# Kernel tuning notes

Hardware: AMD Instinct MI355X
Metric: run time of the kernel (lower is better)

The kernel has to match this reference:

```python
import jax, jax.numpy as jnp
import numpy as np

N, K, D, V = 20000, 16, 256, 64  # nodes, neighbors, embed_dim, edge vocab


def setup_inputs() -> dict:
    key = jax.random.key(0)
    ks = jax.random.split(key, 16)
    s = 1.0 / np.sqrt(2 * D)  # Linear(512 -> 256) init scale
    return {
        "node_reps": jax.random.normal(ks[0], (1, N, D), jnp.float32),
        "in_indices": jax.random.randint(ks[1], (1, N, K), 0, N, jnp.int32),
        "in_edges": jax.random.randint(ks[2], (1, N, K), 0, V, jnp.int32),
        "in_mask": jax.random.uniform(ks[3], (1, N, K), jnp.float32),
        "out_indices": jax.random.randint(ks[4], (1, N, K), 0, N, jnp.int32),
        "out_edges": jax.random.randint(ks[5], (1, N, K), 0, V, jnp.int32),
        "out_mask": jax.random.uniform(ks[6], (1, N, K), jnp.float32),
        "edge_emb_1": jax.random.normal(ks[7], (V, D), jnp.float32),
        "W_1": jax.random.uniform(ks[8], (2 * D, D), jnp.float32, -s, s),
        "b_1": jnp.zeros((D,), jnp.float32),
        "edge_emb_2": jax.random.normal(ks[9], (V, D), jnp.float32),
        "W_2": jax.random.uniform(ks[10], (2 * D, D), jnp.float32, -s, s),
        "b_2": jnp.zeros((D,), jnp.float32),
        "edge_emb_3": jax.random.normal(ks[11], (V, D), jnp.float32),
        "W_3": jax.random.uniform(ks[12], (2 * D, D), jnp.float32, -s, s),
        "b_3": jnp.zeros((D,), jnp.float32),
    }


def gcn_layer(node_reps, in_idx, in_edg, in_msk, out_idx, out_edg, out_msk,
              edge_emb, W, b):
    # node_reps: [1, N, D]; dropout is identity in eval mode.
    nodes = node_reps[0]  # [N, D]; batch_size == 1 as in the original repo

    def agg(idx, edg, msk):
        nbr = nodes[idx]          # gather: [1, N, K, D]
        erep = edge_emb[edg]      # embedding lookup: [1, N, K, D]
        reps = jnp.concatenate([nbr, erep], axis=3) * msk[..., None]
        return reps.sum(axis=2)   # masked sum over neighbors: [1, N, 2D]

    in_reps = agg(in_idx, in_edg, in_msk)
    out_reps = agg(out_idx, out_edg, out_msk)
    in_nodes = in_reps[0] @ W + b    # [N, D]
    out_nodes = out_reps[0] @ W + b  # [N, D]
    return node_reps + out_nodes + in_nodes  # broadcast -> [1, N, D]


def reference(node_reps, in_indices, in_edges, in_mask,
              out_indices, out_edges, out_mask,
              edge_emb_1, W_1, b_1, edge_emb_2, W_2, b_2, edge_emb_3, W_3, b_3):
    nbrs = (in_indices, in_edges, in_mask, out_indices, out_edges, out_mask)
    hidden = gcn_layer(node_reps, *nbrs, edge_emb_1, W_1, b_1)  # gc1
    mu = gcn_layer(hidden, *nbrs, edge_emb_2, W_2, b_2)          # gc2
    logvar = gcn_layer(hidden, *nbrs, edge_emb_3, W_3, b_3)      # gc3

    mu_t = jnp.tanh(mu[0])        # [N, D]
    lv_t = jnp.tanh(logvar[0])    # [N, D]
    n_nodes = mu_t.shape[0]
    kld = (-0.5 / n_nodes) * jnp.mean(
        jnp.sum(1.0 + 2.0 * lv_t - mu_t ** 2 - jnp.exp(lv_t) ** 2, axis=1))
    return hidden, kld
```

## Files before the change

kernel.cpp:

```cpp
#include <hip/hip_runtime.h>
#include <math.h>

#define NN 20000
#define KK 16
#define DD 256
#define VV 64
#define NT1 16
#define SAS 336
#define SAS8 336

typedef __attribute__((ext_vector_type(8))) __bf16 bf16x8;
typedef __attribute__((ext_vector_type(4))) float floatx4;
typedef __attribute__((ext_vector_type(2))) float floatx2;
typedef __attribute__((ext_vector_type(8))) unsigned short ushort8;

__device__ __forceinline__ float4 ld4(const float* p) { return *reinterpret_cast<const float4*>(p); }

__device__ __forceinline__ unsigned short f2bf(float f) {
    union { float f; unsigned u; } v; v.f = f;
    unsigned r = v.u + 0x7FFFu + ((v.u >> 16) & 1u);
    return (unsigned short)(r >> 16);
}
__device__ __forceinline__ float bf2f(unsigned short u) {
    union { unsigned u; float f; } v; v.u = ((unsigned)u) << 16;
    return v.f;
}
__device__ __forceinline__ unsigned char f2q(float f) {
    return (unsigned char)(__builtin_amdgcn_cvt_pk_fp8_f32(f, 0.f, 0u, false) & 0xFFu);
}
__device__ __forceinline__ float q2f(unsigned char q) {
    floatx2 r = __builtin_amdgcn_cvt_pk_f32_fp8((unsigned)q, false);
    return r.x;
}
__device__ __forceinline__ float ftanh(float v) {
    float e = __expf(2.f * v);
    return 1.f - 2.f * __builtin_amdgcn_rcpf(e + 1.f);
}

__global__ __launch_bounds__(256) void setup(
    const int* __restrict__ ie, const float* __restrict__ im,
    const int* __restrict__ oe, const float* __restrict__ om,
    const float* __restrict__ x,
    const float* __restrict__ e1, const float* __restrict__ W1,
    const float* __restrict__ e2, const float* __restrict__ W2,
    const float* __restrict__ e3, const float* __restrict__ W3,
    unsigned short* __restrict__ U1, unsigned char* __restrict__ U23,
    unsigned short* __restrict__ Hc, unsigned char* __restrict__ Hc8,
    unsigned short* __restrict__ xh) {
    int blk = blockIdx.x, tid = threadIdx.x;
    if (blk < 120) {
        int u1path = blk < 40;
        int NT = u1path ? 16 : 32;
        int g = (u1path ? blk : blk - 40) * 256 + tid;
        int lane = g & 63, ntk = g >> 6;
        int nt = ntk % NT, kt = ntk / NT;
        if (kt >= 10) return;
        int n = nt * 16 + (lane & 15);
        int kbase = kt * 32 + (lane >> 4) * 8;
        const float* W; const float* emb;
        if (u1path)       { W = W1; emb = e1; }
        else if (n < 256) { W = W2; emb = e2; }
        else              { W = W3; emb = e3; n -= 256; }
        float vals[8];
        if (kbase < 256) {
            #pragma unroll
            for (int j = 0; j < 8; ++j) vals[j] = W[(size_t)(kbase + j) * DD + n];
        } else {
            int vb = kbase - 256;
            #pragma unroll
            for (int z = 0; z < 8; ++z) vals[z] = 0.f;
            #pragma unroll 4
            for (int j = 0; j < 256; ++j) {
                float wv = W[(size_t)(256 + j) * DD + n];
                #pragma unroll
                for (int z = 0; z < 8; ++z) vals[z] += emb[(vb + z) * DD + j] * wv;
            }
        }
        if (u1path) {
            unsigned short o8[8];
            #pragma unroll
            for (int j = 0; j < 8; ++j) o8[j] = f2bf(vals[j]);
            *reinterpret_cast<uint4*>(&U1[(size_t)g * 8]) = *reinterpret_cast<uint4*>(o8);
        } else {
            unsigned char o8[8];
            #pragma unroll
            for (int j = 0; j < 8; ++j) o8[j] = f2q(vals[j]);
            *reinterpret_cast<uint2*>(&U23[(size_t)g * 8]) = *reinterpret_cast<uint2*>(o8);
        }
    } else {
        int pb = blk - 120;
        int w = tid >> 6, lane = tid & 63;
        int n = pb * 4 + w;
        int e = 0; float m = 0.f;
        if (lane < 16)      { e = ie[n * KK + lane];      m = im[n * KK + lane]; }
        else if (lane < 32) { e = oe[n * KK + lane - 16]; m = om[n * KK + lane - 16]; }
        float h = 0.f;
        #pragma unroll
        for (int j = 0; j < 32; ++j) {
            int ev = __shfl(e, j);
            float mv = __shfl(m, j);
            if (ev == lane) h += mv;
        }
        Hc [(size_t)n * 64 + lane] = f2bf(h);
        Hc8[(size_t)n * 64 + lane] = f2q(h);
        size_t base = (size_t)pb * 1024 + tid * 4;
        float4 v = ld4(x + base);
        ushort4 o; o.x = f2bf(v.x); o.y = f2bf(v.y); o.z = f2bf(v.z); o.w = f2bf(v.w);
        *reinterpret_cast<ushort4*>(xh + base) = o;
    }
}

__global__ __launch_bounds__(256) void fmm1(const unsigned short* __restrict__ xh, const unsigned short* __restrict__ Hc,
                                            const int* __restrict__ ii, const float* __restrict__ im,
                                            const int* __restrict__ oi, const float* __restrict__ om,
                                            const unsigned short* __restrict__ U, const float* __restrict__ b,
                                            float* __restrict__ out, unsigned char* __restrict__ h8) {
    __shared__ unsigned short sA[16 * SAS];
    __shared__ int sidx[16][32];
    __shared__ float smsk[16][32];
    int n0 = blockIdx.x * 16;
    int tid = threadIdx.x;
    for (int q = tid; q < 512; q += 256) {
        int r = q >> 5, j = q & 31;
        int n = n0 + r;
        sidx[r][j] = (j < 16) ? ii[n * KK + j] : oi[n * KK + j - 16];
        smsk[r][j] = (j < 16) ? im[n * KK + j] : om[n * KK + j - 16];
    }
    if (tid < 128) {
        int r = tid >> 3, k8 = tid & 7;
        *reinterpret_cast<uint4*>(&sA[r * SAS + 256 + k8 * 8]) =
            *reinterpret_cast<const uint4*>(&Hc[(size_t)(n0 + r) * 64 + k8 * 8]);
    }
    __syncthreads();
    int lane = tid & 63, w = tid >> 6;
    int half = lane >> 5, c = (lane & 31) * 8;
    #pragma unroll
    for (int rr = 0; rr < 4; ++rr) {
        int row = w * 4 + rr;
        float acc[8] = {0.f, 0.f, 0.f, 0.f, 0.f, 0.f, 0.f, 0.f};
        #pragma unroll
        for (int j = 0; j < 16; ++j) {
            int j2 = j * 2 + half;
            int idx = sidx[row][j2];
            float m = smsk[row][j2];
            ushort8 u = *reinterpret_cast<const ushort8*>(xh + (size_t)idx * DD + c);
            #pragma unroll
            for (int z = 0; z < 8; ++z) acc[z] += m * bf2f(u[z]);
        }
        #pragma unroll
        for (int z = 0; z < 8; ++z) acc[z] += __shfl_xor(acc[z], 32);
        if (half == 0) {
            unsigned short o8[8];
            #pragma unroll
            for (int z = 0; z < 8; ++z) o8[z] = f2bf(acc[z]);
            *reinterpret_cast<uint4*>(&sA[row * SAS + c]) = *reinterpret_cast<uint4*>(o8);
        }
    }
    __syncthreads();
    int lr = lane & 15, quad = lane >> 4;
    float xp[4][4], bb[4];
    #pragma unroll
    for (int t = 0; t < 4; ++t) {
        int col = (w * 4 + t) * 16 + lr;
        bb[t] = 2.f * b[col];
        #pragma unroll
        for (int r = 0; r < 4; ++r)
            xp[t][r] = bf2f(xh[(size_t)(n0 + quad * 4 + r) * DD + col]);
    }
    floatx4 z = {0.f, 0.f, 0.f, 0.f};
    floatx4 acc[4] = {z, z, z, z};
    for (int kt = 0; kt < 10; ++kt) {
        bf16x8 a = *reinterpret_cast<const bf16x8*>(&sA[lr * SAS + kt * 32 + quad * 8]);
        #pragma unroll
        for (int t = 0; t < 4; ++t) {
            bf16x8 bf = *reinterpret_cast<const bf16x8*>(&U[(size_t)((kt * NT1 + w * 4 + t) * 64 + lane) * 8]);
            acc[t] = __builtin_amdgcn_mfma_f32_16x16x32_bf16(a, bf, acc[t], 0, 0, 0);
        }
    }
    #pragma unroll
    for (int t = 0; t < 4; ++t) {
        int col = (w * 4 + t) * 16 + lr;
        #pragma unroll
        for (int r = 0; r < 4; ++r) {
            size_t o = (size_t)(n0 + quad * 4 + r) * DD + col;
            float v = xp[t][r] + bb[t] + acc[t][r];
            out[o] = v;
            h8[o] = f2q(v);
        }
    }
}

__global__ __launch_bounds__(256) void fmm23(const unsigned char* __restrict__ h8, const unsigned char* __restrict__ Hc8,
                                             const int* __restrict__ ii, const float* __restrict__ im,
                                             const int* __restrict__ oi, const float* __restrict__ om,
                                             const unsigned char* __restrict__ U, const float* __restrict__ b2,
                                             const float* __restrict__ b3, float* __restrict__ kld) {
    __shared__ unsigned char sA[16 * SAS8];
    __shared__ int sidx[16][32];
    __shared__ float smsk[16][32];
    __shared__ float red[4];
    int n0 = blockIdx.x * 16;
    int tid = threadIdx.x;
    for (int q = tid; q < 512; q += 256) {
        int r = q >> 5, j = q & 31;
        int n = n0 + r;
        sidx[r][j] = (j < 16) ? ii[n * KK + j] : oi[n * KK + j - 16];
        smsk[r][j] = (j < 16) ? im[n * KK + j] : om[n * KK + j - 16];
    }
    if (tid < 128) {
        int r = tid >> 3, k8 = tid & 7;
        *reinterpret_cast<uint2*>(&sA[r * SAS8 + 256 + k8 * 8]) =
            *reinterpret_cast<const uint2*>(&Hc8[(size_t)(n0 + r) * 64 + k8 * 8]);
    }
    __syncthreads();
    int lane = tid & 63, w = tid >> 6;
    int g = lane >> 4, cl = lane & 15;
    #pragma unroll
    for (int rr = 0; rr < 4; ++rr) {
        int row = w * 4 + rr;
        float acc[16];
        #pragma unroll
        for (int z = 0; z < 16; ++z) acc[z] = 0.f;
        #pragma unroll
        for (int j = 0; j < 8; ++j) {
            int r = g * 8 + j;
            int idx = sidx[row][r];
            float m = smsk[row][r];
            uint4 u = *reinterpret_cast<const uint4*>(h8 + (size_t)idx * DD + cl * 16);
            unsigned dw[4] = {u.x, u.y, u.z, u.w};
            #pragma unroll
            for (int d = 0; d < 4; ++d) {
                floatx2 f01 = __builtin_amdgcn_cvt_pk_f32_fp8(dw[d], false);
                floatx2 f23 = __builtin_amdgcn_cvt_pk_f32_fp8(dw[d], true);
                acc[d * 4 + 0] += m * f01.x; acc[d * 4 + 1] += m * f01.y;
                acc[d * 4 + 2] += m * f23.x; acc[d * 4 + 3] += m * f23.y;
            }
        }
        #pragma unroll
        for (int z = 0; z < 16; ++z) {
            acc[z] += __shfl_xor(acc[z], 16);
            acc[z] += __shfl_xor(acc[z], 32);
        }
        if (g == 0) {
            unsigned char o16[16];
            #pragma unroll
            for (int z = 0; z < 16; ++z) o16[z] = f2q(acc[z]);
            *reinterpret_cast<uint4*>(&sA[row * SAS8 + cl * 16]) = *reinterpret_cast<uint4*>(o16);
        }
    }
    __syncthreads();
    int lr = lane & 15, quad = lane >> 4;
    float hp[4][4], bm[4], bl[4];
    #pragma unroll
    for (int t = 0; t < 4; ++t) {
        int col = (w * 4 + t) * 16 + lr;
        bm[t] = 2.f * b2[col];
        bl[t] = 2.f * b3[col];
        #pragma unroll
        for (int r = 0; r < 4; ++r)
            hp[t][r] = q2f(h8[(size_t)(n0 + quad * 4 + r) * DD + col]);
    }
    floatx4 z = {0.f, 0.f, 0.f, 0.f};
    floatx4 am[4] = {z, z, z, z};
    floatx4 al[4] = {z, z, z, z};
    for (int kt = 0; kt < 10; ++kt) {
        long a = *reinterpret_cast<const long*>(&sA[lr * SAS8 + kt * 32 + quad * 8]);
        #pragma unroll
        for (int t = 0; t < 4; ++t) {
            int nt = w * 4 + t;
            long bmu = *reinterpret_cast<const long*>(&U[(size_t)((kt * 32 + nt) * 64 + lane) * 8]);
            long blv = *reinterpret_cast<const long*>(&U[(size_t)((kt * 32 + 16 + nt) * 64 + lane) * 8]);
            am[t] = __builtin_amdgcn_mfma_f32_16x16x32_fp8_fp8(a, bmu, am[t], 0, 0, 0);
            al[t] = __builtin_amdgcn_mfma_f32_16x16x32_fp8_fp8(a, blv, al[t], 0, 0, 0);
        }
    }
    float kacc = 0.f;
    #pragma unroll
    for (int t = 0; t < 4; ++t) {
        #pragma unroll
        for (int r = 0; r < 4; ++r) {
            float h = hp[t][r];
            float tm = ftanh(h + bm[t] + am[t][r]);
            float tl = ftanh(h + bl[t] + al[t][r]);
            kacc += (1.f - tm * tm) + (2.f * tl - __expf(2.f * tl));
        }
    }
    #pragma unroll
    for (int off = 32; off > 0; off >>= 1) kacc += __shfl_xor(kacc, off);
    if (lane == 0) red[w] = kacc;
    __syncthreads();
    if (tid == 0)
        atomicAdd(kld, (red[0] + red[1] + red[2] + red[3]) * (-0.5f / ((float)NN * (float)NN)));
}

extern "C" void kernel_launch(void* const* d_in, const int* in_sizes, int n_in,
                              void* d_out, int out_size, void* d_ws, size_t ws_size,
                              hipStream_t stream) {
    const float* x  = (const float*)d_in[0];
    const int*   ii = (const int*)d_in[1];
    const int*   ie = (const int*)d_in[2];
    const float* im = (const float*)d_in[3];
    const int*   oi = (const int*)d_in[4];
    const int*   oe = (const int*)d_in[5];
    const float* om = (const float*)d_in[6];
    const float* e1 = (const float*)d_in[7];
    const float* W1 = (const float*)d_in[8];
    const float* b1 = (const float*)d_in[9];
    const float* e2 = (const float*)d_in[10];
    const float* W2 = (const float*)d_in[11];
    const float* b2 = (const float*)d_in[12];
    const float* e3 = (const float*)d_in[13];
    const float* W3 = (const float*)d_in[14];
    const float* b3 = (const float*)d_in[15];
    float* out = (float*)d_out;

    char* ws = (char*)d_ws;
    unsigned short* U1  = (unsigned short*)(ws);
    unsigned char*  U23 = (unsigned char*)(ws + 163840);
    unsigned short* Hc  = (unsigned short*)(ws + 327680);
    unsigned char*  Hc8 = (unsigned char*)(ws + 2887680);
    unsigned short* xh  = (unsigned short*)(ws + 4167680);
    unsigned char*  h8  = (unsigned char*)(ws + 14407680);

    hipMemsetAsync(out + (size_t)NN * DD, 0, 4, stream);
    setup<<<120 + NN / 4, 256, 0, stream>>>(ie, im, oe, om, x, e1, W1, e2, W2, e3, W3,
                                            U1, U23, Hc, Hc8, xh);
    fmm1 <<<NN / 16, 256, 0, stream>>>(xh, Hc, ii, im, oi, om, U1, b1, out, h8);
    fmm23<<<NN / 16, 256, 0, stream>>>(h8, Hc8, ii, im, oi, om, U23, b2, b3,
                                       out + (size_t)NN * DD);
}
```

Measured before the change: 202.0 us.

## Split fused gather+GEMM into column-chunked aggregation kernels and separate 32-row MFMA kernels

Splits each fused gather-then-GEMM kernel into two launches. The first is an aggregation kernel that gathers neighbor rows in column chunks, so each block touches only a slice of the feature table, and writes a bf16 aggregate buffer. The second is a GEMM kernel that processes 32 rows per block and reuses each B fragment across two M tiles. Layers 2/3 switch from fp8 to bf16 for the aggregate and weights, and nontemporal loads/stores are used for the intermediates. This aims to improve cache locality of the random gathers and MFMA reuse, at the cost of extra kernel launches and a round trip of the aggregate buffer through global memory.

```diff
diff --git a/kernel.cpp b/kernel.cpp
--- a/kernel.cpp
+++ b/kernel.cpp
@@ -5,14 +5,14 @@
 #define KK 16
 #define DD 256
 #define VV 64
-#define NT1 16
 #define SAS 336
-#define SAS8 336
 
 typedef __attribute__((ext_vector_type(8))) __bf16 bf16x8;
 typedef __attribute__((ext_vector_type(4))) float floatx4;
 typedef __attribute__((ext_vector_type(2))) float floatx2;
 typedef __attribute__((ext_vector_type(8))) unsigned short ushort8;
+typedef __attribute__((ext_vector_type(4))) unsigned int uint4v;
+typedef __attribute__((ext_vector_type(2))) unsigned int uint2v;
 
 __device__ __forceinline__ float4 ld4(const float* p) { return *reinterpret_cast<const float4*>(p); }
 
@@ -44,9 +44,8 @@
     const float* __restrict__ e1, const float* __restrict__ W1,
     const float* __restrict__ e2, const float* __restrict__ W2,
     const float* __restrict__ e3, const float* __restrict__ W3,
-    unsigned short* __restrict__ U1, unsigned char* __restrict__ U23,
-    unsigned short* __restrict__ Hc, unsigned char* __restrict__ Hc8,
-    unsigned short* __restrict__ xh) {
+    unsigned short* __restrict__ U1, unsigned short* __restrict__ U23,
+    unsigned short* __restrict__ Sb, unsigned short* __restrict__ xh) {
     int blk = blockIdx.x, tid = threadIdx.x;
     if (blk < 120) {
         int u1path = blk < 40;
@@ -76,17 +75,11 @@
                 for (int z = 0; z < 8; ++z) vals[z] += emb[(vb + z) * DD + j] * wv;
             }
         }
-        if (u1path) {
-            unsigned short o8[8];
-            #pragma unroll
-            for (int j = 0; j < 8; ++j) o8[j] = f2bf(vals[j]);
-            *reinterpret_cast<uint4*>(&U1[(size_t)g * 8]) = *reinterpret_cast<uint4*>(o8);
-        } else {
-            unsigned char o8[8];
-            #pragma unroll
-            for (int j = 0; j < 8; ++j) o8[j] = f2q(vals[j]);
-            *reinterpret_cast<uint2*>(&U23[(size_t)g * 8]) = *reinterpret_cast<uint2*>(o8);
-        }
+        unsigned short o8[8];
+        #pragma unroll
+        for (int j = 0; j < 8; ++j) o8[j] = f2bf(vals[j]);
+        unsigned short* U = u1path ? U1 : U23;
+        *reinterpret_cast<uint4v*>(&U[(size_t)g * 8]) = *reinterpret_cast<uint4v*>(o8);
     } else {
         int pb = blk - 120;
         int w = tid >> 6, lane = tid & 63;
@@ -101,8 +94,7 @@
             float mv = __shfl(m, j);
             if (ev == lane) h += mv;
         }
-        Hc [(size_t)n * 64 + lane] = f2bf(h);
-        Hc8[(size_t)n * 64 + lane] = f2q(h);
+        Sb[(size_t)n * 320 + 256 + lane] = f2bf(h);
         size_t base = (size_t)pb * 1024 + tid * 4;
         float4 v = ld4(x + base);
         ushort4 o; o.x = f2bf(v.x); o.y = f2bf(v.y); o.z = f2bf(v.z); o.w = f2bf(v.w);
@@ -110,179 +102,203 @@
     }
 }
 
-__global__ __launch_bounds__(256) void fmm1(const unsigned short* __restrict__ xh, const unsigned short* __restrict__ Hc,
+__global__ __launch_bounds__(256) void aggx(const unsigned short* __restrict__ xh,
                                             const int* __restrict__ ii, const float* __restrict__ im,
                                             const int* __restrict__ oi, const float* __restrict__ om,
-                                            const unsigned short* __restrict__ U, const float* __restrict__ b,
-                                            float* __restrict__ out, unsigned char* __restrict__ h8) {
-    __shared__ unsigned short sA[16 * SAS];
-    __shared__ int sidx[16][32];
-    __shared__ float smsk[16][32];
-    int n0 = blockIdx.x * 16;
+                                            unsigned short* __restrict__ Sb) {
+    int blk = blockIdx.x;
+    int chunk = blk / 2500, nb = blk % 2500;
+    int w = threadIdx.x >> 6, lane = threadIdx.x & 63;
+    int na = nb * 8 + w * 2, nbod = na + 1;
+    int rg = lane >> 3, co = lane & 7;
+    const unsigned short* base = xh + chunk * 64 + co * 8;
+    float acc[2][8];
+    #pragma unroll
+    for (int s = 0; s < 2; ++s)
+        #pragma unroll
+        for (int z = 0; z < 8; ++z) acc[s][z] = 0.f;
+    #pragma unroll
+    for (int s = 0; s < 2; ++s) {
+        int n = s ? nbod : na;
+        int i0 = ii[n * KK + rg], i1 = ii[n * KK + rg + 8];
+        int i2 = oi[n * KK + rg], i3 = oi[n * KK + rg + 8];
+        float m0 = im[n * KK + rg], m1 = im[n * KK + rg + 8];
+        float m2 = om[n * KK + rg], m3 = om[n * KK + rg + 8];
+        ushort8 u0 = *reinterpret_cast<const ushort8*>(base + (size_t)i0 * DD);
+        ushort8 u1 = *reinterpret_cast<const ushort8*>(base + (size_t)i1 * DD);
+        ushort8 u2 = *reinterpret_cast<const ushort8*>(base + (size_t)i2 * DD);
+        ushort8 u3 = *reinterpret_cast<const ushort8*>(base + (size_t)i3 * DD);
+        #pragma unroll
+        for (int z = 0; z < 8; ++z)
+            acc[s][z] = m0 * bf2f(u0[z]) + m1 * bf2f(u1[z]) + m2 * bf2f(u2[z]) + m3 * bf2f(u3[z]);
+    }
+    #pragma unroll
+    for (int s = 0; s < 2; ++s)
+        #pragma unroll
+        for (int z = 0; z < 8; ++z) {
+            acc[s][z] += __shfl_xor(acc[s][z], 8);
+            acc[s][z] += __shfl_xor(acc[s][z], 16);
+            acc[s][z] += __shfl_xor(acc[s][z], 32);
+        }
+    if (rg < 2) {
+        int n = rg ? nbod : na;
+        unsigned short o8[8];
+        #pragma unroll
+        for (int z = 0; z < 8; ++z) o8[z] = f2bf(acc[rg][z]);
+        __builtin_nontemporal_store(*reinterpret_cast<uint4v*>(o8),
+            reinterpret_cast<uint4v*>(&Sb[(size_t)n * 320 + chunk * 64 + co * 8]));
+    }
+}
+
+__global__ __launch_bounds__(256) void aggq(const unsigned char* __restrict__ h8,
+                                            const int* __restrict__ ii, const float* __restrict__ im,
+                                            const int* __restrict__ oi, const float* __restrict__ om,
+                                            unsigned short* __restrict__ Sb) {
+    int blk = blockIdx.x;
+    int chunk = blk / 2500, nb = blk % 2500;
+    int w = threadIdx.x >> 6, lane = threadIdx.x & 63;
+    int na = nb * 8 + w * 2, nbod = na + 1;
+    int rg = lane >> 3, co = lane & 7;
+    const unsigned char* base = h8 + chunk * 128 + co * 16;
+    float acc[2][16];
+    #pragma unroll
+    for (int s = 0; s < 2; ++s)
+        #pragma unroll
+        for (int z = 0; z < 16; ++z) acc[s][z] = 0.f;
+    #pragma unroll
+    for (int s = 0; s < 2; ++s) {
+        int n = s ? nbod : na;
+        int idx[4]; float msk[4];
+        idx[0] = ii[n * KK + rg]; idx[1] = ii[n * KK + rg + 8];
+        idx[2] = oi[n * KK + rg]; idx[3] = oi[n * KK + rg + 8];
+        msk[0] = im[n * KK + rg]; msk[1] = im[n * KK + rg + 8];
+        msk[2] = om[n * KK + rg]; msk[3] = om[n * KK + rg + 8];
+        #pragma unroll
+        for (int j = 0; j < 4; ++j) {
+            uint4v u = *reinterpret_cast<const uint4v*>(base + (size_t)idx[j] * DD);
+            float m = msk[j];
+            #pragma unroll
+            for (int d = 0; d < 4; ++d) {
+                floatx2 f01 = __builtin_amdgcn_cvt_pk_f32_fp8(u[d], false);
+                floatx2 f23 = __builtin_amdgcn_cvt_pk_f32_fp8(u[d], true);
+                acc[s][d * 4 + 0] += m * f01.x; acc[s][d * 4 + 1] += m * f01.y;
+                acc[s][d * 4 + 2] += m * f23.x; acc[s][d * 4 + 3] += m * f23.y;
+            }
+        }
+    }
+    #pragma unroll
+    for (int s = 0; s < 2; ++s)
+        #pragma unroll
+        for (int z = 0; z < 16; ++z) {
+            acc[s][z] += __shfl_xor(acc[s][z], 8);
+            acc[s][z] += __shfl_xor(acc[s][z], 16);
+            acc[s][z] += __shfl_xor(acc[s][z], 32);
+        }
+    if (rg < 2) {
+        int n = rg ? nbod : na;
+        unsigned short o16[16];
+        #pragma unroll
+        for (int z = 0; z < 16; ++z) o16[z] = f2bf(acc[rg][z]);
+        uint4v* dst = reinterpret_cast<uint4v*>(&Sb[(size_t)n * 320 + chunk * 128 + co * 16]);
+        __builtin_nontemporal_store(reinterpret_cast<uint4v*>(o16)[0], dst);
+        __builtin_nontemporal_store(reinterpret_cast<uint4v*>(o16)[1], dst + 1);
+    }
+}
+
+__global__ __launch_bounds__(256) void mm1(const unsigned short* __restrict__ Sb, const unsigned short* __restrict__ U,
+                                           const unsigned short* __restrict__ xh, const float* __restrict__ b,
+                                           float* __restrict__ out, unsigned char* __restrict__ h8) {
+    __shared__ unsigned short sA[32 * SAS];
+    int n0 = blockIdx.x * 32;
     int tid = threadIdx.x;
-    for (int q = tid; q < 512; q += 256) {
-        int r = q >> 5, j = q & 31;
-        int n = n0 + r;
-        sidx[r][j] = (j < 16) ? ii[n * KK + j] : oi[n * KK + j - 16];
-        smsk[r][j] = (j < 16) ? im[n * KK + j] : om[n * KK + j - 16];
-    }
-    if (tid < 128) {
-        int r = tid >> 3, k8 = tid & 7;
-        *reinterpret_cast<uint4*>(&sA[r * SAS + 256 + k8 * 8]) =
-            *reinterpret_cast<const uint4*>(&Hc[(size_t)(n0 + r) * 64 + k8 * 8]);
+    #pragma unroll
+    for (int q = 0; q < 5; ++q) {
+        int c = q * 256 + tid;
+        int row = c / 40, k8 = c % 40;
+        *reinterpret_cast<uint4v*>(&sA[row * SAS + k8 * 8]) = __builtin_nontemporal_load(
+            reinterpret_cast<const uint4v*>(&Sb[(size_t)(n0 + row) * 320 + k8 * 8]));
     }
     __syncthreads();
     int lane = tid & 63, w = tid >> 6;
-    int half = lane >> 5, c = (lane & 31) * 8;
-    #pragma unroll
-    for (int rr = 0; rr < 4; ++rr) {
-        int row = w * 4 + rr;
-        float acc[8] = {0.f, 0.f, 0.f, 0.f, 0.f, 0.f, 0.f, 0.f};
-        #pragma unroll
-        for (int j = 0; j < 16; ++j) {
-            int j2 = j * 2 + half;
-            int idx = sidx[row][j2];
-            float m = smsk[row][j2];
-            ushort8 u = *reinterpret_cast<const ushort8*>(xh + (size_t)idx * DD + c);
-            #pragma unroll
-            for (int z = 0; z < 8; ++z) acc[z] += m * bf2f(u[z]);
-        }
-        #pragma unroll
-        for (int z = 0; z < 8; ++z) acc[z] += __shfl_xor(acc[z], 32);
-        if (half == 0) {
-            unsigned short o8[8];
-            #pragma unroll
-            for (int z = 0; z < 8; ++z) o8[z] = f2bf(acc[z]);
-            *reinterpret_cast<uint4*>(&sA[row * SAS + c]) = *reinterpret_cast<uint4*>(o8);
-        }
-    }
-    __syncthreads();
     int lr = lane & 15, quad = lane >> 4;
-    float xp[4][4], bb[4];
+    floatx4 z = {0.f, 0.f, 0.f, 0.f};
+    floatx4 acc[2][4] = {{z, z, z, z}, {z, z, z, z}};
+    for (int kt = 0; kt < 10; ++kt) {
+        bf16x8 a0 = *reinterpret_cast<const bf16x8*>(&sA[lr * SAS + kt * 32 + quad * 8]);
+        bf16x8 a1 = *reinterpret_cast<const bf16x8*>(&sA[(lr + 16) * SAS + kt * 32 + quad * 8]);
+        #pragma unroll
+        for (int t = 0; t < 4; ++t) {
+            bf16x8 bf = *reinterpret_cast<const bf16x8*>(&U[(size_t)((kt * 16 + w * 4 + t) * 64 + lane) * 8]);
+            acc[0][t] = __builtin_amdgcn_mfma_f32_16x16x32_bf16(a0, bf, acc[0][t], 0, 0, 0);
+            acc[1][t] = __builtin_amdgcn_mfma_f32_16x16x32_bf16(a1, bf, acc[1][t], 0, 0, 0);
+        }
+    }
     #pragma unroll
     for (int t = 0; t < 4; ++t) {
         int col = (w * 4 + t) * 16 + lr;
-        bb[t] = 2.f * b[col];
-        #pragma unroll
-        for (int r = 0; r < 4; ++r)
-            xp[t][r] = bf2f(xh[(size_t)(n0 + quad * 4 + r) * DD + col]);
-    }
+        float bb = 2.f * b[col];
+        #pragma unroll
+        for (int mt = 0; mt < 2; ++mt) {
+            #pragma unroll
+            for (int r = 0; r < 4; ++r) {
+                size_t o = (size_t)(n0 + mt * 16 + quad * 4 + r) * DD + col;
+                float v = bf2f(xh[o]) + bb + acc[mt][t][r];
+                __builtin_nontemporal_store(v, out + o);
+                h8[o] = f2q(v);
+            }
+        }
+    }
+}
+
+__global__ __launch_bounds__(256) void mm23(const unsigned short* __restrict__ Sb, const unsigned short* __restrict__ U,
+                                            const unsigned char* __restrict__ h8, const float* __restrict__ b2,
+                                            const float* __restrict__ b3, float* __restrict__ kld) {
+    __shared__ unsigned short sA[32 * SAS];
+    __shared__ float red[4];
+    int n0 = blockIdx.x * 32;
+    int tid = threadIdx.x;
+    #pragma unroll
+    for (int q = 0; q < 5; ++q) {
+        int c = q * 256 + tid;
+        int row = c / 40, k8 = c % 40;
+        *reinterpret_cast<uint4v*>(&sA[row * SAS + k8 * 8]) = __builtin_nontemporal_load(
+            reinterpret_cast<const uint4v*>(&Sb[(size_t)(n0 + row) * 320 + k8 * 8]));
+    }
+    __syncthreads();
+    int lane = tid & 63, w = tid >> 6;
+    int lr = lane & 15, quad = lane >> 4;
     floatx4 z = {0.f, 0.f, 0.f, 0.f};
-    floatx4 acc[4] = {z, z, z, z};
+    floatx4 am[2][4] = {{z, z, z, z}, {z, z, z, z}};
+    floatx4 al[2][4] = {{z, z, z, z}, {z, z, z, z}};
     for (int kt = 0; kt < 10; ++kt) {
-        bf16x8 a = *reinterpret_cast<const bf16x8*>(&sA[lr * SAS + kt * 32 + quad * 8]);
+        bf16x8 a0 = *reinterpret_cast<const bf16x8*>(&sA[lr * SAS + kt * 32 + quad * 8]);
+        bf16x8 a1 = *reinterpret_cast<const bf16x8*>(&sA[(lr + 16) * SAS + kt * 32 + quad * 8]);
         #pragma unroll
         for (int t = 0; t < 4; ++t) {
-            bf16x8 bf = *reinterpret_cast<const bf16x8*>(&U[(size_t)((kt * NT1 + w * 4 + t) * 64 + lane) * 8]);
-            acc[t] = __builtin_amdgcn_mfma_f32_16x16x32_bf16(a, bf, acc[t], 0, 0, 0);
-        }
-    }
+            int nt = w * 4 + t;
+            bf16x8 bmu = *reinterpret_cast<const bf16x8*>(&U[(size_t)((kt * 32 + nt) * 64 + lane) * 8]);
+            bf16x8 blv = *reinterpret_cast<const bf16x8*>(&U[(size_t)((kt * 32 + 16 + nt) * 64 + lane) * 8]);
+            am[0][t] = __builtin_amdgcn_mfma_f32_16x16x32_bf16(a0, bmu, am[0][t], 0, 0, 0);
+            am[1][t] = __builtin_amdgcn_mfma_f32_16x16x32_bf16(a1, bmu, am[1][t], 0, 0, 0);
+            al[0][t] = __builtin_amdgcn_mfma_f32_16x16x32_bf16(a0, blv, al[0][t], 0, 0, 0);
+            al[1][t] = __builtin_amdgcn_mfma_f32_16x16x32_bf16(a1, blv, al[1][t], 0, 0, 0);
+        }
+    }
+    float kacc = 0.f;
     #pragma unroll
     for (int t = 0; t < 4; ++t) {
         int col = (w * 4 + t) * 16 + lr;
-        #pragma unroll
-        for (int r = 0; r < 4; ++r) {
-            size_t o = (size_t)(n0 + quad * 4 + r) * DD + col;
-            float v = xp[t][r] + bb[t] + acc[t][r];
-            out[o] = v;
-            h8[o] = f2q(v);
-        }
-    }
-}
-
-__global__ __launch_bounds__(256) void fmm23(const unsigned char* __restrict__ h8, const unsigned char* __restrict__ Hc8,
-                                             const int* __restrict__ ii, const float* __restrict__ im,
-                                             const int* __restrict__ oi, const float* __restrict__ om,
-                                             const unsigned char* __restrict__ U, const float* __restrict__ b2,
-                                             const float* __restrict__ b3, float* __restrict__ kld) {
-    __shared__ unsigned char sA[16 * SAS8];
-    __shared__ int sidx[16][32];
-    __shared__ float smsk[16][32];
-    __shared__ float red[4];
-    int n0 = blockIdx.x * 16;
-    int tid = threadIdx.x;
-    for (int q = tid; q < 512; q += 256) {
-        int r = q >> 5, j = q & 31;
-        int n = n0 + r;
-        sidx[r][j] = (j < 16) ? ii[n * KK + j] : oi[n * KK + j - 16];
-        smsk[r][j] = (j < 16) ? im[n * KK + j] : om[n * KK + j - 16];
-    }
-    if (tid < 128) {
-        int r = tid >> 3, k8 = tid & 7;
-        *reinterpret_cast<uint2*>(&sA[r * SAS8 + 256 + k8 * 8]) =
-            *reinterpret_cast<const uint2*>(&Hc8[(size_t)(n0 + r) * 64 + k8 * 8]);
-    }
-    __syncthreads();
-    int lane = tid & 63, w = tid >> 6;
-    int g = lane >> 4, cl = lane & 15;
-    #pragma unroll
-    for (int rr = 0; rr < 4; ++rr) {
-        int row = w * 4 + rr;
-        float acc[16];
-        #pragma unroll
-        for (int z = 0; z < 16; ++z) acc[z] = 0.f;
-        #pragma unroll
-        for (int j = 0; j < 8; ++j) {
-            int r = g * 8 + j;
-            int idx = sidx[row][r];
-            float m = smsk[row][r];
-            uint4 u = *reinterpret_cast<const uint4*>(h8 + (size_t)idx * DD + cl * 16);
-            unsigned dw[4] = {u.x, u.y, u.z, u.w};
-            #pragma unroll
-            for (int d = 0; d < 4; ++d) {
-                floatx2 f01 = __builtin_amdgcn_cvt_pk_f32_fp8(dw[d], false);
-                floatx2 f23 = __builtin_amdgcn_cvt_pk_f32_fp8(dw[d], true);
-                acc[d * 4 + 0] += m * f01.x; acc[d * 4 + 1] += m * f01.y;
-                acc[d * 4 + 2] += m * f23.x; acc[d * 4 + 3] += m * f23.y;
+        float bm = 2.f * b2[col];
+        float bl = 2.f * b3[col];
+        #pragma unroll
+        for (int mt = 0; mt < 2; ++mt) {
+            #pragma unroll
+            for (int r = 0; r < 4; ++r) {
+                float h = q2f(h8[(size_t)(n0 + mt * 16 + quad * 4 + r) * DD + col]);
+                float tm = ftanh(h + bm + am[mt][t][r]);
+                float tl = ftanh(h + bl + al[mt][t][r]);
+                kacc += (1.f - tm * tm) + (2.f * tl - __expf(2.f * tl));
             }
-        }
-        #pragma unroll
-        for (int z = 0; z < 16; ++z) {
-            acc[z] += __shfl_xor(acc[z], 16);
-            acc[z] += __shfl_xor(acc[z], 32);
-        }
-        if (g == 0) {
-            unsigned char o16[16];
-            #pragma unroll
-            for (int z = 0; z < 16; ++z) o16[z] = f2q(acc[z]);
-            *reinterpret_cast<uint4*>(&sA[row * SAS8 + cl * 16]) = *reinterpret_cast<uint4*>(o16);
-        }
-    }
-    __syncthreads();
-    int lr = lane & 15, quad = lane >> 4;
-    float hp[4][4], bm[4], bl[4];
-    #pragma unroll
-    for (int t = 0; t < 4; ++t) {
-        int col = (w * 4 + t) * 16 + lr;
-        bm[t] = 2.f * b2[col];
-        bl[t] = 2.f * b3[col];
-        #pragma unroll
-        for (int r = 0; r < 4; ++r)
-            hp[t][r] = q2f(h8[(size_t)(n0 + quad * 4 + r) * DD + col]);
-    }
-    floatx4 z = {0.f, 0.f, 0.f, 0.f};
-    floatx4 am[4] = {z, z, z, z};
-    floatx4 al[4] = {z, z, z, z};
-    for (int kt = 0; kt < 10; ++kt) {
-        long a = *reinterpret_cast<const long*>(&sA[lr * SAS8 + kt * 32 + quad * 8]);
-        #pragma unroll
-        for (int t = 0; t < 4; ++t) {
-            int nt = w * 4 + t;
-            long bmu = *reinterpret_cast<const long*>(&U[(size_t)((kt * 32 + nt) * 64 + lane) * 8]);
-            long blv = *reinterpret_cast<const long*>(&U[(size_t)((kt * 32 + 16 + nt) * 64 + lane) * 8]);
-            am[t] = __builtin_amdgcn_mfma_f32_16x16x32_fp8_fp8(a, bmu, am[t], 0, 0, 0);
-            al[t] = __builtin_amdgcn_mfma_f32_16x16x32_fp8_fp8(a, blv, al[t], 0, 0, 0);
-        }
-    }
-    float kacc = 0.f;
-    #pragma unroll
-    for (int t = 0; t < 4; ++t) {
-        #pragma unroll
-        for (int r = 0; r < 4; ++r) {
-            float h = hp[t][r];
-            float tm = ftanh(h + bm[t] + am[t][r]);
-            float tl = ftanh(h + bl[t] + al[t][r]);
-            kacc += (1.f - tm * tm) + (2.f * tl - __expf(2.f * tl));
         }
     }
     #pragma unroll
@@ -316,16 +332,17 @@
 
     char* ws = (char*)d_ws;
     unsigned short* U1  = (unsigned short*)(ws);
-    unsigned char*  U23 = (unsigned char*)(ws + 163840);
-    unsigned short* Hc  = (unsigned short*)(ws + 327680);
-    unsigned char*  Hc8 = (unsigned char*)(ws + 2887680);
-    unsigned short* xh  = (unsigned short*)(ws + 4167680);
-    unsigned char*  h8  = (unsigned char*)(ws + 14407680);
-
-    hipMemsetAsync(out + (size_t)NN * DD, 0, 4, stream);
+    unsigned short* U23 = (unsigned short*)(ws + 163840);
+    unsigned short* Sb  = (unsigned short*)(ws + 491520);
+    unsigned short* xh  = (unsigned short*)(ws + 13291520);
+    unsigned char*  h8  = (unsigned char*)(ws + 23531520);
+
+    (void)hipMemsetAsync(out + (size_t)NN * DD, 0, 4, stream);
     setup<<<120 + NN / 4, 256, 0, stream>>>(ie, im, oe, om, x, e1, W1, e2, W2, e3, W3,
-                                            U1, U23, Hc, Hc8, xh);
-    fmm1 <<<NN / 16, 256, 0, stream>>>(xh, Hc, ii, im, oi, om, U1, b1, out, h8);
-    fmm23<<<NN / 16, 256, 0, stream>>>(h8, Hc8, ii, im, oi, om, U23, b2, b3,
+                                            U1, U23, Sb, xh);
+    aggx <<<4 * NN / 8, 256, 0, stream>>>(xh, ii, im, oi, om, Sb);
+    mm1  <<<NN / 32, 256, 0, stream>>>(Sb, U1, xh, b1, out, h8);
+    aggq <<<2 * NN / 8, 256, 0, stream>>>(h8, ii, im, oi, om, Sb);
+    mm23 <<<NN / 32, 256, 0, stream>>>(Sb, U23, h8, b2, b3,
                                        out + (size_t)NN * DD);
 }
```

Result: slower. 250.9 us (+24.3%).
